# Performance work log

Hardware: AMD Instinct MI355X
Metric: run time of the kernel (lower is better)

Reference implementation:

```python
import jax, jax.numpy as jnp
import numpy as np

B, S, D, H = 8, 2048, 1024, 64

def setup_inputs() -> dict:
    key = jax.random.key(0)
    k1, k2, k3, k4 = jax.random.split(key, 4)
    idx = jax.random.normal(k1, (B, S, D), dtype=jnp.float32)
    # nn.Linear(D, H, bias=False) weights, stored as [D, H] for x @ W
    Wk = jax.random.normal(k2, (D, H), dtype=jnp.float32) * (1.0 / np.sqrt(D))
    Wq = jax.random.normal(k3, (D, H), dtype=jnp.float32) * (1.0 / np.sqrt(D))
    Wv = jax.random.normal(k4, (D, H), dtype=jnp.float32) * (1.0 / np.sqrt(D))
    return {"idx": idx, "Wk": Wk, "Wq": Wq, "Wv": Wv}

def reference(idx, Wk, Wq, Wv):
    b, s, d = idx.shape
    k = idx @ Wk  # [b, s, h]
    q = idx @ Wq
    v = idx @ Wv
    # NOTE: original scales by embedding_dim**-0.5, not head_size**-0.5
    wei = jnp.einsum('bqh,bkh->bqk', q, k) * (d ** -0.5)
    causal = jnp.tril(jnp.ones((s, s), dtype=bool))
    wei = jnp.where(causal, wei, -jnp.inf)
    attn = jax.nn.softmax(wei, axis=-1)  # dropout p=0.0 -> identity
    return jnp.einsum('bqk,bkh->bqh', attn, v)
```

## Files before the change

### kernel.cpp

```cpp
#include <hip/hip_runtime.h>

typedef __attribute__((ext_vector_type(8))) short short8;
typedef __attribute__((ext_vector_type(4))) float f32x4;

#define MFMA_16x16x32_BF16(A, B, C) __builtin_amdgcn_mfma_f32_16x16x32_bf16(A, B, C, 0, 0, 0)

__device__ __forceinline__ unsigned short f2bf(float x) {
    unsigned int u = __builtin_bit_cast(unsigned int, x);
    u = (u + 0x7FFFu + ((u >> 16) & 1u)) >> 16;
    return (unsigned short)u;
}

__global__ __launch_bounds__(256) void wconv_kernel(const float* __restrict__ Wk,
                                                    const float* __restrict__ Wq,
                                                    const float* __restrict__ Wv,
                                                    unsigned short* __restrict__ Wt) {
    const int n = blockIdx.x;
    const float* W = (n < 64) ? Wk : (n < 128) ? Wq : Wv;
    const int col = n & 63;
    const int sw = (n & 7) << 3;
    for (int k = threadIdx.x; k < 1024; k += 256) {
        const int kd = (k & ~56) | ((k ^ sw) & 56);
        Wt[(size_t)n * 1024 + kd] = f2bf(W[(size_t)k * 64 + col]);
    }
}

__global__ __launch_bounds__(512, 4) void proj_kernel(const float* __restrict__ X,
                                                      const unsigned short* __restrict__ Wt,
                                                      unsigned short* __restrict__ Kb,
                                                      unsigned short* __restrict__ Qb,
                                                      unsigned short* __restrict__ Vt2) {
    __shared__ __attribute__((aligned(16))) unsigned short Wl[2][192 * 64];
    __shared__ __attribute__((aligned(16))) unsigned short Al[2][32 * 72];
    const int t = threadIdx.x;
    const int w = t >> 6, lane = t & 63, lr = lane & 15, g = lane >> 4;
    const int rw = w >> 2, cw = w & 3;
    const int r0 = blockIdx.x * 32;

    f32x4 acc[3] = {};

    const int ar = t >> 4, ac = (t & 15) * 4;
    const float* xsrc = X + (size_t)(r0 + ar) * 1024 + ac;

    float4 fly = *(const float4*)xsrc;
    uint2 aw;
    aw.x = (unsigned)f2bf(fly.x) | ((unsigned)f2bf(fly.y) << 16);
    aw.y = (unsigned)f2bf(fly.z) | ((unsigned)f2bf(fly.w) << 16);
    *(uint2*)&Al[0][ar * 72 + ac] = aw;
#pragma unroll
    for (int i = 0; i < 3; ++i) {
        const int q = t + 512 * i;
        const unsigned short* src = Wt + (size_t)(q >> 3) * 1024 + (q & 7) * 8;
        __builtin_amdgcn_global_load_lds((const __attribute__((address_space(1))) void*)src,
                                         (__attribute__((address_space(3))) void*)&Wl[0][q * 8],
                                         16, 0, 0);
    }
    __builtin_amdgcn_sched_barrier(0);
    fly = *(const float4*)(xsrc + 64);
    asm volatile("s_waitcnt vmcnt(1) lgkmcnt(0)" ::: "memory");
    __builtin_amdgcn_s_barrier();

    for (int t16 = 0; t16 < 16; ++t16) {
        const int cur = t16 & 1;
        if (t16 < 15) {
            aw.x = (unsigned)f2bf(fly.x) | ((unsigned)f2bf(fly.y) << 16);
            aw.y = (unsigned)f2bf(fly.z) | ((unsigned)f2bf(fly.w) << 16);
            *(uint2*)&Al[cur ^ 1][ar * 72 + ac] = aw;
            const int k1 = (t16 + 1) * 64;
#pragma unroll
            for (int i = 0; i < 3; ++i) {
                const int q = t + 512 * i;
                const unsigned short* src = Wt + (size_t)(q >> 3) * 1024 + k1 + (q & 7) * 8;
                __builtin_amdgcn_global_load_lds((const __attribute__((address_space(1))) void*)src,
                                                 (__attribute__((address_space(3))) void*)&Wl[cur ^ 1][q * 8],
                                                 16, 0, 0);
            }
            __builtin_amdgcn_sched_barrier(0);
            const int anext = (t16 + 2 < 15) ? (t16 + 2) : 15;
            fly = *(const float4*)(xsrc + anext * 64);
        }

        short8 af[2];
        af[0] = *(const short8*)&Al[cur][(16 * rw + lr) * 72 + 8 * g];
        af[1] = *(const short8*)&Al[cur][(16 * rw + lr) * 72 + 32 + 8 * g];
#pragma unroll
        for (int c = 0; c < 3; ++c) {
            const int row = 48 * cw + 16 * c + lr;
#pragma unroll
            for (int sub = 0; sub < 2; ++sub) {
                const int cs = (4 * sub + g) ^ (lr & 7);
                short8 wf = *(const short8*)&Wl[cur][row * 64 + cs * 8];
                acc[c] = MFMA_16x16x32_BF16(af[sub], wf, acc[c]);
            }
        }
        asm volatile("s_waitcnt vmcnt(1) lgkmcnt(0)" ::: "memory");
        __builtin_amdgcn_s_barrier();
    }

    const int bb = r0 >> 11;
    const int row = r0 + 16 * rw + 4 * g;
#pragma unroll
    for (int i = 0; i < 3; ++i) {
        const int cg = cw * 3 + i;
        if (cg < 4) {
#pragma unroll
            for (int r = 0; r < 4; ++r)
                Kb[(size_t)(row + r) * 64 + 16 * cg + lr] = f2bf(acc[i][r]);
        } else if (cg < 8) {
#pragma unroll
            for (int r = 0; r < 4; ++r)
                Qb[(size_t)(row + r) * 64 + 16 * (cg - 4) + lr] = f2bf(acc[i][r]);
        } else {
            const int h = 16 * (cg - 8) + lr;
            uint2 e;
            e.x = (unsigned)f2bf(acc[i][0]) | ((unsigned)f2bf(acc[i][1]) << 16);
            e.y = (unsigned)f2bf(acc[i][2]) | ((unsigned)f2bf(acc[i][3]) << 16);
            *(uint2*)(Vt2 + (size_t)bb * 64 * 2048 + (size_t)h * 2048
                      + ((r0 & 2047) >> 5) * 32 + g * 8 + 4 * rw) = e;
        }
    }
}

__global__ __launch_bounds__(512, 2) void attn_kernel(const unsigned short* __restrict__ Kb,
                                                      const unsigned short* __restrict__ Qb,
                                                      const unsigned short* __restrict__ Vt2,
                                                      float* __restrict__ out) {
    __shared__ __attribute__((aligned(16))) float Pacc[16][32][68];
    __shared__ float Pml[2][16][32];

    const int t = threadIdx.x;
    const int w = t >> 6, lane = t & 63;
    const int lr = lane & 15, g = lane >> 4;
    const int p = blockIdx.x, b = blockIdx.y;
    const int nhi = 64 - p;
    const int q0h = (63 - p) * 32, q0l = p * 32;
    const size_t rowbase = (size_t)b * 2048;
    const size_t vbase = (size_t)b * 64 * 2048;
    const float NEG_INF = -__builtin_inff();
    const float SCALE2 = 0.03125f * 1.4426950408889634f;

    short8 qfH[2][2], qfL[2][2];
#pragma unroll
    for (int sub = 0; sub < 2; ++sub)
#pragma unroll
        for (int hh = 0; hh < 2; ++hh) {
            qfH[sub][hh] = *(const short8*)(Qb + (rowbase + q0h + 16 * sub + lr) * 64 + 32 * hh + 8 * g);
            qfL[sub][hh] = *(const short8*)(Qb + (rowbase + q0l + 16 * sub + lr) * 64 + 32 * hh + 8 * g);
        }

    f32x4 accH[2][4] = {}, accL[2][4] = {};
    float mH[2] = {NEG_INF, NEG_INF}, mL[2] = {NEG_INF, NEG_INF};
    float lH[2] = {0.f, 0.f}, lL[2] = {0.f, 0.f};

    const int s0 = (w * 65) >> 3, s1 = ((w + 1) * 65) >> 3;

    auto loadS = [&](int kv0, short8 (&kf)[2][2], short8 (&vf)[4]) {
#pragma unroll
        for (int f = 0; f < 2; ++f)
#pragma unroll
            for (int hh = 0; hh < 2; ++hh)
                kf[f][hh] = *(const short8*)(Kb + (rowbase + kv0 + 16 * f + lr) * 64 + 32 * hh + 8 * g);
#pragma unroll
        for (int fh = 0; fh < 4; ++fh)
            vf[fh] = *(const short8*)(Vt2 + vbase + (size_t)(16 * fh + lr) * 2048 + (kv0 >> 5) * 32 + 8 * g);
    };

    auto comp = [&](int kv0, int q0, const short8 (&qf)[2][2],
                    const short8 (&kf)[2][2], const short8 (&vf)[4],
                    f32x4 (&acc)[2][4], float (&m2)[2], float (&ls)[2]) {
#pragma unroll
        for (int sub = 0; sub < 2; ++sub) {
            f32x4 sv[2];
#pragma unroll
            for (int f = 0; f < 2; ++f) {
                f32x4 x = {};
                x = MFMA_16x16x32_BF16(kf[f][0], qf[sub][0], x);
                x = MFMA_16x16x32_BF16(kf[f][1], qf[sub][1], x);
                sv[f] = x;
            }
            const int q = q0 + 16 * sub + lr;
            float pvv[8], tmax = NEG_INF;
#pragma unroll
            for (int f = 0; f < 2; ++f)
#pragma unroll
                for (int r = 0; r < 4; ++r) {
                    int kp = kv0 + 16 * f + 4 * g + r;
                    float sc = sv[f][r] * SCALE2;
                    sc = (kp <= q) ? sc : NEG_INF;
                    pvv[4 * f + r] = sc;
                    tmax = fmaxf(tmax, sc);
                }
            tmax = fmaxf(tmax, __shfl_xor(tmax, 16));
            tmax = fmaxf(tmax, __shfl_xor(tmax, 32));
            float mnew = fmaxf(m2[sub], tmax);
            float alpha = exp2f(m2[sub] - mnew);
            float psum = 0.f;
            short8 pf;
#pragma unroll
            for (int e = 0; e < 8; ++e) {
                float pe = exp2f(pvv[e] - mnew);
                psum += pe;
                pf[e] = (short)f2bf(pe);
            }
            psum += __shfl_xor(psum, 16);
            psum += __shfl_xor(psum, 32);
            ls[sub] = ls[sub] * alpha + psum;
            m2[sub] = mnew;
#pragma unroll
            for (int fh = 0; fh < 4; ++fh) {
                acc[sub][fh][0] *= alpha; acc[sub][fh][1] *= alpha;
                acc[sub][fh][2] *= alpha; acc[sub][fh][3] *= alpha;
                acc[sub][fh] = MFMA_16x16x32_BF16(vf[fh], pf, acc[sub][fh]);
            }
        }
    };

    short8 kfA[2][2], vfA[4], kfB[2][2], vfB[4];

    {
        const int e = (s1 < nhi) ? s1 : nhi;
        int s = s0;
        for (; s + 1 < e; s += 2) {
            loadS(s * 32, kfA, vfA);
            loadS((s + 1) * 32, kfB, vfB);
            comp(s * 32, q0h, qfH, kfA, vfA, accH, mH, lH);
            comp((s + 1) * 32, q0h, qfH, kfB, vfB, accH, mH, lH);
        }
        if (s < e) {
            loadS(s * 32, kfA, vfA);
            comp(s * 32, q0h, qfH, kfA, vfA, accH, mH, lH);
        }
    }
    {
        int s = (s0 > nhi) ? s0 : nhi;
        for (; s + 1 < s1; s += 2) {
            loadS((s - nhi) * 32, kfA, vfA);
            loadS((s + 1 - nhi) * 32, kfB, vfB);
            comp((s - nhi) * 32, q0l, qfL, kfA, vfA, accL, mL, lL);
            comp((s + 1 - nhi) * 32, q0l, qfL, kfB, vfB, accL, mL, lL);
        }
        if (s < s1) {
            loadS((s - nhi) * 32, kfA, vfA);
            comp((s - nhi) * 32, q0l, qfL, kfA, vfA, accL, mL, lL);
        }
    }

#pragma unroll
    for (int bnd = 0; bnd < 2; ++bnd) {
        const f32x4 (&acc)[2][4] = bnd ? accL : accH;
        const float (&m2)[2] = bnd ? mL : mH;
        const float (&ls)[2] = bnd ? lL : lH;
        const int slot = bnd * 8 + w;
#pragma unroll
        for (int sub = 0; sub < 2; ++sub) {
#pragma unroll
            for (int fh = 0; fh < 4; ++fh)
                *(f32x4*)&Pacc[slot][16 * sub + lr][16 * fh + 4 * g] = acc[sub][fh];
            if (g == 0) {
                Pml[0][slot][16 * sub + lr] = m2[sub];
                Pml[1][slot][16 * sub + lr] = ls[sub];
            }
        }
    }
    __syncthreads();

    {
        const int tb = t >> 8, t2 = t & 255;
        const int qq = t2 & 31, hb = (t2 >> 5) * 8;
        float mw[8], M = NEG_INF;
#pragma unroll
        for (int wv = 0; wv < 8; ++wv) {
            mw[wv] = Pml[0][tb * 8 + wv][qq];
            M = fmaxf(M, mw[wv]);
        }
        float wgt[8], L = 0.f;
#pragma unroll
        for (int wv = 0; wv < 8; ++wv) {
            wgt[wv] = exp2f(mw[wv] - M);
            L += wgt[wv] * Pml[1][tb * 8 + wv][qq];
        }
        f32x4 o0 = {}, o1 = {};
#pragma unroll
        for (int wv = 0; wv < 8; ++wv) {
            f32x4 a0 = *(const f32x4*)&Pacc[tb * 8 + wv][qq][hb];
            f32x4 a1 = *(const f32x4*)&Pacc[tb * 8 + wv][qq][hb + 4];
            o0 += wgt[wv] * a0;
            o1 += wgt[wv] * a1;
        }
        const float invL = 1.f / L;
        o0 *= invL; o1 *= invL;
        const int q0 = tb ? q0l : q0h;
        float* op = out + (rowbase + q0 + qq) * 64 + hb;
        *(f32x4*)op = o0;
        *(f32x4*)(op + 4) = o1;
    }
}

extern "C" void kernel_launch(void* const* d_in, const int* in_sizes, int n_in,
                              void* d_out, int out_size, void* d_ws, size_t ws_size,
                              hipStream_t stream) {
    const float* X  = (const float*)d_in[0];
    const float* Wk = (const float*)d_in[1];
    const float* Wq = (const float*)d_in[2];
    const float* Wv = (const float*)d_in[3];

    unsigned short* Wt  = (unsigned short*)d_ws;
    unsigned short* Kb  = Wt + 192 * 1024;
    unsigned short* Qb  = Kb + 16384 * 64;
    unsigned short* Vt2 = Qb + 16384 * 64;
    float* out = (float*)d_out;

    wconv_kernel<<<dim3(192), dim3(256), 0, stream>>>(Wk, Wq, Wv, Wt);
    proj_kernel<<<dim3(512), dim3(512), 0, stream>>>(X, Wt, Kb, Qb, Vt2);
    attn_kernel<<<dim3(32, 8), dim3(512), 0, stream>>>(Kb, Qb, Vt2, out);
}
```

Baseline: 49.03 us.

## Pre-convert X to swizzled bf16 and stage it into LDS via direct loads

Adds a standalone kernel that converts the fp32 input to bf16 in a swizzled layout in workspace, and the projection kernel then loads A tiles with global_load_lds instead of converting in registers. The aim is to simplify the projection inner loop and avoid register staging and LDS padding. In exchange it adds an extra kernel launch and extra global traffic (writing and re-reading a bf16 copy of X). It also replaces the fine-grained vmcnt waits with full __syncthreads, which may reduce prefetch overlap.

```diff
diff --git a/kernel.cpp b/kernel.cpp
--- a/kernel.cpp
+++ b/kernel.cpp
@@ -25,13 +25,35 @@
     }
 }
 
-__global__ __launch_bounds__(512, 4) void proj_kernel(const float* __restrict__ X,
+__global__ __launch_bounds__(256) void xconv_kernel(const float* __restrict__ X,
+                                                    unsigned short* __restrict__ Xb) {
+    const int t = threadIdx.x;
+    const size_t base = (size_t)blockIdx.x * 4 * 1024;
+#pragma unroll
+    for (int i = 0; i < 2; ++i) {
+        const int q = t + 256 * i;
+        const int row = q >> 7, c = q & 127;
+        const float* src = X + base + (size_t)row * 1024 + c * 8;
+        float4 v0 = *(const float4*)src;
+        float4 v1 = *(const float4*)(src + 4);
+        uint4 o;
+        o.x = (unsigned)f2bf(v0.x) | ((unsigned)f2bf(v0.y) << 16);
+        o.y = (unsigned)f2bf(v0.z) | ((unsigned)f2bf(v0.w) << 16);
+        o.z = (unsigned)f2bf(v1.x) | ((unsigned)f2bf(v1.y) << 16);
+        o.w = (unsigned)f2bf(v1.z) | ((unsigned)f2bf(v1.w) << 16);
+        const int kt = c >> 3, cl = c & 7;
+        const int arow = (blockIdx.x * 4 + row) & 7;
+        *(uint4*)&Xb[base + (size_t)row * 1024 + kt * 64 + (cl ^ arow) * 8] = o;
+    }
+}
+
+__global__ __launch_bounds__(512, 2) void proj_kernel(const unsigned short* __restrict__ Xb,
                                                       const unsigned short* __restrict__ Wt,
                                                       unsigned short* __restrict__ Kb,
                                                       unsigned short* __restrict__ Qb,
                                                       unsigned short* __restrict__ Vt2) {
     __shared__ __attribute__((aligned(16))) unsigned short Wl[2][192 * 64];
-    __shared__ __attribute__((aligned(16))) unsigned short Al[2][32 * 72];
+    __shared__ __attribute__((aligned(16))) unsigned short Al[2][32 * 64];
     const int t = threadIdx.x;
     const int w = t >> 6, lane = t & 63, lr = lane & 15, g = lane >> 4;
     const int rw = w >> 2, cw = w & 3;
@@ -39,50 +61,38 @@
 
     f32x4 acc[3] = {};
 
-    const int ar = t >> 4, ac = (t & 15) * 4;
-    const float* xsrc = X + (size_t)(r0 + ar) * 1024 + ac;
-
-    float4 fly = *(const float4*)xsrc;
-    uint2 aw;
-    aw.x = (unsigned)f2bf(fly.x) | ((unsigned)f2bf(fly.y) << 16);
-    aw.y = (unsigned)f2bf(fly.z) | ((unsigned)f2bf(fly.w) << 16);
-    *(uint2*)&Al[0][ar * 72 + ac] = aw;
-#pragma unroll
-    for (int i = 0; i < 3; ++i) {
-        const int q = t + 512 * i;
-        const unsigned short* src = Wt + (size_t)(q >> 3) * 1024 + (q & 7) * 8;
-        __builtin_amdgcn_global_load_lds((const __attribute__((address_space(1))) void*)src,
-                                         (__attribute__((address_space(3))) void*)&Wl[0][q * 8],
-                                         16, 0, 0);
-    }
-    __builtin_amdgcn_sched_barrier(0);
-    fly = *(const float4*)(xsrc + 64);
-    asm volatile("s_waitcnt vmcnt(1) lgkmcnt(0)" ::: "memory");
-    __builtin_amdgcn_s_barrier();
+    auto STAGE = [&](int buf, int t16) {
+        const int k0 = t16 * 64;
+#pragma unroll
+        for (int i = 0; i < 3; ++i) {
+            const int q = t + 512 * i;
+            const unsigned short* src = Wt + (size_t)(q >> 3) * 1024 + k0 + (q & 7) * 8;
+            __builtin_amdgcn_global_load_lds((const __attribute__((address_space(1))) void*)src,
+                                             (__attribute__((address_space(3))) void*)&Wl[buf][q * 8],
+                                             16, 0, 0);
+        }
+        if (t < 256) {
+            const int row = t >> 3, cl = t & 7;
+            const unsigned short* src = Xb + (size_t)(r0 + row) * 1024 + k0 + cl * 8;
+            __builtin_amdgcn_global_load_lds((const __attribute__((address_space(1))) void*)src,
+                                             (__attribute__((address_space(3))) void*)&Al[buf][t * 8],
+                                             16, 0, 0);
+        }
+    };
+
+    STAGE(0, 0);
+    __syncthreads();
 
     for (int t16 = 0; t16 < 16; ++t16) {
         const int cur = t16 & 1;
-        if (t16 < 15) {
-            aw.x = (unsigned)f2bf(fly.x) | ((unsigned)f2bf(fly.y) << 16);
-            aw.y = (unsigned)f2bf(fly.z) | ((unsigned)f2bf(fly.w) << 16);
-            *(uint2*)&Al[cur ^ 1][ar * 72 + ac] = aw;
-            const int k1 = (t16 + 1) * 64;
-#pragma unroll
-            for (int i = 0; i < 3; ++i) {
-                const int q = t + 512 * i;
-                const unsigned short* src = Wt + (size_t)(q >> 3) * 1024 + k1 + (q & 7) * 8;
-                __builtin_amdgcn_global_load_lds((const __attribute__((address_space(1))) void*)src,
-                                                 (__attribute__((address_space(3))) void*)&Wl[cur ^ 1][q * 8],
-                                                 16, 0, 0);
-            }
-            __builtin_amdgcn_sched_barrier(0);
-            const int anext = (t16 + 2 < 15) ? (t16 + 2) : 15;
-            fly = *(const float4*)(xsrc + anext * 64);
-        }
+        if (t16 < 15) STAGE(cur ^ 1, t16 + 1);
 
         short8 af[2];
-        af[0] = *(const short8*)&Al[cur][(16 * rw + lr) * 72 + 8 * g];
-        af[1] = *(const short8*)&Al[cur][(16 * rw + lr) * 72 + 32 + 8 * g];
+#pragma unroll
+        for (int sub = 0; sub < 2; ++sub) {
+            const int cs = (4 * sub + g) ^ (lr & 7);
+            af[sub] = *(const short8*)&Al[cur][(16 * rw + lr) * 64 + cs * 8];
+        }
 #pragma unroll
         for (int c = 0; c < 3; ++c) {
             const int row = 48 * cw + 16 * c + lr;
@@ -93,8 +103,7 @@
                 acc[c] = MFMA_16x16x32_BF16(af[sub], wf, acc[c]);
             }
         }
-        asm volatile("s_waitcnt vmcnt(1) lgkmcnt(0)" ::: "memory");
-        __builtin_amdgcn_s_barrier();
+        if (t16 < 15) __syncthreads();
     }
 
     const int bb = r0 >> 11;
@@ -303,14 +312,16 @@
     const float* Wk = (const float*)d_in[1];
     const float* Wq = (const float*)d_in[2];
     const float* Wv = (const float*)d_in[3];
+    float* out = (float*)d_out;
 
     unsigned short* Wt  = (unsigned short*)d_ws;
-    unsigned short* Kb  = Wt + 192 * 1024;
+    unsigned short* Xb  = Wt + 192 * 1024;
+    unsigned short* Kb  = Xb + (size_t)16384 * 1024;
     unsigned short* Qb  = Kb + 16384 * 64;
     unsigned short* Vt2 = Qb + 16384 * 64;
-    float* out = (float*)d_out;
 
     wconv_kernel<<<dim3(192), dim3(256), 0, stream>>>(Wk, Wq, Wv, Wt);
-    proj_kernel<<<dim3(512), dim3(512), 0, stream>>>(X, Wt, Kb, Qb, Vt2);
+    xconv_kernel<<<dim3(4096), dim3(256), 0, stream>>>(X, Xb);
+    proj_kernel<<<dim3(512), dim3(512), 0, stream>>>(Xb, Wt, Kb, Qb, Vt2);
     attn_kernel<<<dim3(32, 8), dim3(512), 0, stream>>>(Kb, Qb, Vt2, out);
 }
```

Result: slower. 60.22 us (+22.8%).

## Split projection output columns across two blocks with 256-thread blocks

Applied to the files above, without the earlier changes.

The projection kernel now launches 1024 blocks of 256 threads. Each block computes 32 rows by 96 of the 192 output columns instead of all 192, so the per-block LDS weight tile is halved and more blocks run in flight. The price is that each X row tile is read and converted to bf16 twice, once per column half, which doubles global reads of X. The hand-written waitcnt and s_barrier pairs are replaced with plain __syncthreads, which may lose some load overlap.

```diff
diff --git a/kernel.cpp b/kernel.cpp
--- a/kernel.cpp
+++ b/kernel.cpp
@@ -25,67 +25,77 @@
     }
 }
 
-__global__ __launch_bounds__(512, 4) void proj_kernel(const float* __restrict__ X,
+__global__ __launch_bounds__(256, 4) void proj_kernel(const float* __restrict__ X,
                                                       const unsigned short* __restrict__ Wt,
                                                       unsigned short* __restrict__ Kb,
                                                       unsigned short* __restrict__ Qb,
                                                       unsigned short* __restrict__ Vt2) {
-    __shared__ __attribute__((aligned(16))) unsigned short Wl[2][192 * 64];
+    __shared__ __attribute__((aligned(16))) unsigned short Wl[2][96 * 64];
     __shared__ __attribute__((aligned(16))) unsigned short Al[2][32 * 72];
     const int t = threadIdx.x;
     const int w = t >> 6, lane = t & 63, lr = lane & 15, g = lane >> 4;
-    const int rw = w >> 2, cw = w & 3;
-    const int r0 = blockIdx.x * 32;
+    const int wr = w >> 1, wc = w & 1;
+    const int rt = blockIdx.x >> 1, cb = blockIdx.x & 1;
+    const int r0 = rt * 32;
+    const int n0 = cb * 96;
 
     f32x4 acc[3] = {};
 
-    const int ar = t >> 4, ac = (t & 15) * 4;
-    const float* xsrc = X + (size_t)(r0 + ar) * 1024 + ac;
-
-    float4 fly = *(const float4*)xsrc;
-    uint2 aw;
-    aw.x = (unsigned)f2bf(fly.x) | ((unsigned)f2bf(fly.y) << 16);
-    aw.y = (unsigned)f2bf(fly.z) | ((unsigned)f2bf(fly.w) << 16);
-    *(uint2*)&Al[0][ar * 72 + ac] = aw;
+    const int ar = t >> 3, aj = t & 7;
+    const float* xsrc = X + (size_t)(r0 + ar) * 1024 + aj * 8;
+
+    {
+        float4 f0 = *(const float4*)xsrc;
+        float4 f1 = *(const float4*)(xsrc + 4);
+        uint4 aw;
+        aw.x = (unsigned)f2bf(f0.x) | ((unsigned)f2bf(f0.y) << 16);
+        aw.y = (unsigned)f2bf(f0.z) | ((unsigned)f2bf(f0.w) << 16);
+        aw.z = (unsigned)f2bf(f1.x) | ((unsigned)f2bf(f1.y) << 16);
+        aw.w = (unsigned)f2bf(f1.z) | ((unsigned)f2bf(f1.w) << 16);
+        *(uint4*)&Al[0][ar * 72 + aj * 8] = aw;
+    }
 #pragma unroll
     for (int i = 0; i < 3; ++i) {
-        const int q = t + 512 * i;
-        const unsigned short* src = Wt + (size_t)(q >> 3) * 1024 + (q & 7) * 8;
+        const int q = t + 256 * i;
+        const unsigned short* src = Wt + (size_t)(n0 + (q >> 3)) * 1024 + (q & 7) * 8;
         __builtin_amdgcn_global_load_lds((const __attribute__((address_space(1))) void*)src,
                                          (__attribute__((address_space(3))) void*)&Wl[0][q * 8],
                                          16, 0, 0);
     }
-    __builtin_amdgcn_sched_barrier(0);
-    fly = *(const float4*)(xsrc + 64);
-    asm volatile("s_waitcnt vmcnt(1) lgkmcnt(0)" ::: "memory");
-    __builtin_amdgcn_s_barrier();
+    float4 fly0 = *(const float4*)(xsrc + 64);
+    float4 fly1 = *(const float4*)(xsrc + 68);
+    __syncthreads();
 
     for (int t16 = 0; t16 < 16; ++t16) {
         const int cur = t16 & 1;
         if (t16 < 15) {
-            aw.x = (unsigned)f2bf(fly.x) | ((unsigned)f2bf(fly.y) << 16);
-            aw.y = (unsigned)f2bf(fly.z) | ((unsigned)f2bf(fly.w) << 16);
-            *(uint2*)&Al[cur ^ 1][ar * 72 + ac] = aw;
+            uint4 aw;
+            aw.x = (unsigned)f2bf(fly0.x) | ((unsigned)f2bf(fly0.y) << 16);
+            aw.y = (unsigned)f2bf(fly0.z) | ((unsigned)f2bf(fly0.w) << 16);
+            aw.z = (unsigned)f2bf(fly1.x) | ((unsigned)f2bf(fly1.y) << 16);
+            aw.w = (unsigned)f2bf(fly1.z) | ((unsigned)f2bf(fly1.w) << 16);
+            *(uint4*)&Al[cur ^ 1][ar * 72 + aj * 8] = aw;
             const int k1 = (t16 + 1) * 64;
 #pragma unroll
             for (int i = 0; i < 3; ++i) {
-                const int q = t + 512 * i;
-                const unsigned short* src = Wt + (size_t)(q >> 3) * 1024 + k1 + (q & 7) * 8;
+                const int q = t + 256 * i;
+                const unsigned short* src = Wt + (size_t)(n0 + (q >> 3)) * 1024 + k1 + (q & 7) * 8;
                 __builtin_amdgcn_global_load_lds((const __attribute__((address_space(1))) void*)src,
                                                  (__attribute__((address_space(3))) void*)&Wl[cur ^ 1][q * 8],
                                                  16, 0, 0);
             }
-            __builtin_amdgcn_sched_barrier(0);
-            const int anext = (t16 + 2 < 15) ? (t16 + 2) : 15;
-            fly = *(const float4*)(xsrc + anext * 64);
+            if (t16 < 14) {
+                fly0 = *(const float4*)(xsrc + (t16 + 2) * 64);
+                fly1 = *(const float4*)(xsrc + (t16 + 2) * 64 + 4);
+            }
         }
 
         short8 af[2];
-        af[0] = *(const short8*)&Al[cur][(16 * rw + lr) * 72 + 8 * g];
-        af[1] = *(const short8*)&Al[cur][(16 * rw + lr) * 72 + 32 + 8 * g];
+        af[0] = *(const short8*)&Al[cur][(16 * wr + lr) * 72 + 8 * g];
+        af[1] = *(const short8*)&Al[cur][(16 * wr + lr) * 72 + 32 + 8 * g];
 #pragma unroll
         for (int c = 0; c < 3; ++c) {
-            const int row = 48 * cw + 16 * c + lr;
+            const int row = 48 * wc + 16 * c + lr;
 #pragma unroll
             for (int sub = 0; sub < 2; ++sub) {
                 const int cs = (4 * sub + g) ^ (lr & 7);
@@ -93,15 +103,14 @@
                 acc[c] = MFMA_16x16x32_BF16(af[sub], wf, acc[c]);
             }
         }
-        asm volatile("s_waitcnt vmcnt(1) lgkmcnt(0)" ::: "memory");
-        __builtin_amdgcn_s_barrier();
+        if (t16 < 15) __syncthreads();
     }
 
     const int bb = r0 >> 11;
-    const int row = r0 + 16 * rw + 4 * g;
+    const int row = r0 + 16 * wr + 4 * g;
 #pragma unroll
     for (int i = 0; i < 3; ++i) {
-        const int cg = cw * 3 + i;
+        const int cg = cb * 6 + wc * 3 + i;
         if (cg < 4) {
 #pragma unroll
             for (int r = 0; r < 4; ++r)
@@ -116,7 +125,7 @@
             e.x = (unsigned)f2bf(acc[i][0]) | ((unsigned)f2bf(acc[i][1]) << 16);
             e.y = (unsigned)f2bf(acc[i][2]) | ((unsigned)f2bf(acc[i][3]) << 16);
             *(uint2*)(Vt2 + (size_t)bb * 64 * 2048 + (size_t)h * 2048
-                      + ((r0 & 2047) >> 5) * 32 + g * 8 + 4 * rw) = e;
+                      + ((r0 & 2047) >> 5) * 32 + g * 8 + 4 * wr) = e;
         }
     }
 }
@@ -311,6 +320,6 @@
     float* out = (float*)d_out;
 
     wconv_kernel<<<dim3(192), dim3(256), 0, stream>>>(Wk, Wq, Wv, Wt);
-    proj_kernel<<<dim3(512), dim3(512), 0, stream>>>(X, Wt, Kb, Qb, Vt2);
+    proj_kernel<<<dim3(1024), dim3(256), 0, stream>>>(X, Wt, Kb, Qb, Vt2);
     attn_kernel<<<dim3(32, 8), dim3(512), 0, stream>>>(Kb, Qb, Vt2, out);
 }
```

New measurement: 58.89 us. +20.1%, slower.
